# Kernel optimization log

Hardware: AMD Instinct MI355X
Metric: run time of the kernel (lower is better)

Reference implementation:

```python
import jax, jax.numpy as jnp
import numpy as np

N_NODES = 100000
N_EDGES = 1600000
IN_DIM = 3
LATENT = 128
LATENT_DEC = 128
NUM_LAYER = 2      # shared-weight middle GCN layers
NUM_LAYER_DEC = 2  # shared-weight middle decoder layers


def _glorot(key, shape):
    fan_in, fan_out = shape[0], shape[1]
    lim = np.sqrt(6.0 / (fan_in + fan_out)).astype(np.float32)
    return jax.random.uniform(key, shape, jnp.float32, -lim, lim)


def setup_inputs() -> dict:
    key = jax.random.key(0)
    ks = jax.random.split(key, 10)
    x = jax.random.normal(ks[0], (N_NODES, IN_DIM), jnp.float32)
    edge_index = jax.random.randint(ks[1], (2, N_EDGES), 0, N_NODES, jnp.int64)
    return {
        "x": x,
        "edge_index": edge_index,
        "W_s": _glorot(ks[2], (IN_DIM, LATENT)),   "b_s": jnp.zeros((LATENT,), jnp.float32),
        "W_m": _glorot(ks[3], (LATENT, LATENT)),   "b_m": jnp.zeros((LATENT,), jnp.float32),
        "W_e": _glorot(ks[4], (LATENT, LATENT)),   "b_e": jnp.zeros((LATENT,), jnp.float32),
        "W_sd": _glorot(ks[5], (LATENT, LATENT_DEC)),    "b_sd": jnp.zeros((LATENT_DEC,), jnp.float32),
        "W_md": _glorot(ks[6], (LATENT_DEC, LATENT_DEC)),"b_md": jnp.zeros((LATENT_DEC,), jnp.float32),
        "W_ed": _glorot(ks[7], (LATENT_DEC, IN_DIM)),    "b_ed": jnp.zeros((IN_DIM,), jnp.float32),
    }


def _gcn_conv(h, W, b, src, dst, dinv):
    # PyG GCNConv: out_i = sum_j norm_ij * (x_j @ W) + b, norm = d^-1/2_i d^-1/2_j
    h = h @ W
    norm = dinv[src] * dinv[dst]                       # [E+N]
    msg = norm[:, None] * h[src]                       # gather + scale
    out = jax.ops.segment_sum(msg, dst, num_segments=N_NODES)  # scatter-add
    return out + b


def reference(x, edge_index, W_s, b_s, W_m, b_m, W_e, b_e, W_sd, b_sd, W_md, b_md, W_ed, b_ed):
    loops = jnp.arange(N_NODES, dtype=edge_index.dtype)
    src = jnp.concatenate([edge_index[0], loops])      # add self-loops
    dst = jnp.concatenate([edge_index[1], loops])
    deg = jax.ops.segment_sum(jnp.ones(src.shape[0], x.dtype), dst, num_segments=N_NODES)
    dinv = jnp.where(deg > 0, jax.lax.rsqrt(deg), 0.0)

    h = jax.nn.relu(_gcn_conv(x, W_s, b_s, src, dst, dinv))
    for _ in range(NUM_LAYER):  # shared weights (ModuleList([layer]*n))
        h = jax.nn.relu(_gcn_conv(h, W_m, b_m, src, dst, dinv))
    h = jax.nn.relu(_gcn_conv(h, W_e, b_e, src, dst, dinv))

    h = jax.nn.relu(h @ W_sd + b_sd)
    for _ in range(NUM_LAYER_DEC):  # shared weights
        h = jax.nn.relu(h @ W_md + b_md)
    y = h @ W_ed + b_ed
    return y + x
```

## Files before the change

kernel.cpp:

```cpp
#include <hip/hip_runtime.h>


typedef __attribute__((ext_vector_type(8))) short short8;
typedef __attribute__((ext_vector_type(4))) float floatx4;
typedef __attribute__((ext_vector_type(2))) float floatx2;

#define BIN_CH 8192
#define NBMAX 512
#define BKT 256
#define HS_STRIDE 68

__device__ __forceinline__ unsigned short f2bf(float f) {
    unsigned int u = __float_as_uint(f);
    u += 0x7fffu + ((u >> 16) & 1u);
    return (unsigned short)(u >> 16);
}
__device__ __forceinline__ unsigned int pk_bf(float a, float b) {
    return (unsigned int)f2bf(a) | ((unsigned int)f2bf(b) << 16);
}
__device__ __forceinline__ unsigned char f2fp8(float f) {
    return (unsigned char)(__builtin_amdgcn_cvt_pk_fp8_f32(f, f, 0, false) & 0xFF);
}
__device__ __forceinline__ short8 ld_frag(const unsigned short* p) {
    uint2 a = *(const uint2*)p;
    uint2 b = *(const uint2*)(p + 4);
    int4 v = make_int4((int)a.x, (int)a.y, (int)b.x, (int)b.y);
    return __builtin_bit_cast(short8, v);
}


__global__ void pack_kernel(const float* __restrict__ W0, const float* __restrict__ W1,
                            const float* __restrict__ W2, const float* __restrict__ W3,
                            unsigned short* __restrict__ P0, unsigned short* __restrict__ P1,
                            unsigned short* __restrict__ P2, unsigned short* __restrict__ P3,
                            int* __restrict__ gfill, unsigned char* __restrict__ t8zrow,
                            int NB) {
    if (blockIdx.x == 0) {
        for (int i = threadIdx.x; i < NB; i += 256) gfill[i] = 0;
        if (threadIdx.x < 32) ((unsigned int*)t8zrow)[threadIdx.x] = 0;
    }
    int which = blockIdx.x >> 3;
    const float* W = which == 0 ? W0 : which == 1 ? W1 : which == 2 ? W2 : W3;
    unsigned short* P = which == 0 ? P0 : which == 1 ? P1 : which == 2 ? P2 : P3;
    int f = (blockIdx.x & 7) * 256 + threadIdx.x;
    int lane = f & 63, nt = (f >> 6) & 7, kc = f >> 9;
    int kbase = kc * 32 + (lane >> 4) * 8;
    int ncol = nt * 16 + (lane & 15);
    short8 frag;
    #pragma unroll
    for (int j = 0; j < 8; ++j)
        frag[j] = (short)f2bf(W[(size_t)(kbase + j) * 128 + ncol]);
    *((short8*)(P + (size_t)f * 8)) = frag;
}


__global__ __launch_bounds__(512) void bin_kernel(
        const int* __restrict__ src, const int* __restrict__ dst,
        int* __restrict__ gfill, unsigned int* __restrict__ binbuf,
        int NB, int C, int E) {
    __shared__ int h4[4][NBMAX];
    __shared__ int start[NBMAX];
    __shared__ int tot[NBMAX];
    __shared__ int dstoff[NBMAX];
    int tid = threadIdx.x;
    int grp = tid >> 7;
    int e0 = blockIdx.x * BIN_CH;
    for (int i = tid; i < 4 * NBMAX; i += 512) ((int*)h4)[i] = 0;
    __syncthreads();
    for (int i = tid; i < BIN_CH; i += 512) {
        int e = e0 + i;
        if (e < E) atomicAdd(&h4[grp][dst[e] >> 8], 1);
    }
    __syncthreads();
    if (tid < 64) {
        int carry = 0;
        for (int base = 0; base < NB; base += 64) {
            int idx = base + tid;
            int c0 = 0, c1 = 0, c2 = 0, c3 = 0, v = 0;
            if (idx < NB) {
                c0 = h4[0][idx]; c1 = h4[1][idx];
                c2 = h4[2][idx]; c3 = h4[3][idx];
                v = c0 + c1 + c2 + c3;
            }
            int s = v;
            #pragma unroll
            for (int off = 1; off < 64; off <<= 1) {
                int u = __shfl_up(s, off);
                if (tid >= off) s += u;
            }
            if (idx < NB) {
                int ex = carry + s - v;
                start[idx] = ex;
                tot[idx] = v;
                h4[0][idx] = ex;
                h4[1][idx] = ex + c0;
                h4[2][idx] = ex + c0 + c1;
                h4[3][idx] = ex + c0 + c1 + c2;
            }
            carry += __shfl(s, 63);
        }
    }
    __syncthreads();
    for (int i = tid; i < NB; i += 512) {
        int cnt = tot[i];
        int g = cnt ? atomicAdd(&gfill[i], cnt) : 0;
        dstoff[i] = g - start[i];
    }
    __syncthreads();
    for (int i = tid; i < BIN_CH; i += 512) {
        int e = e0 + i;
        if (e >= E) continue;
        int d = dst[e];
        int b = d >> 8;
        int slot = atomicAdd(&h4[grp][b], 1);
        int gidx = b * C + dstoff[b] + slot;
        if (gidx < (b + 1) * C)
            binbuf[gidx] = (unsigned int)src[e] | ((unsigned int)(d & 255) << 17);
    }
}

__global__ __launch_bounds__(256) void build_kernel(
        const unsigned int* __restrict__ binbuf, const int* __restrict__ gfill,
        int* __restrict__ rowptr, float* __restrict__ dinv, int* __restrict__ col,
        int NB, int C, int N, int E) {
    __shared__ int h4[4][BKT];
    __shared__ int hs[BKT];
    __shared__ int tot[BKT];
    __shared__ int bbase_s;
    int b = blockIdx.x, tid = threadIdx.x;
    int grp = tid >> 6;
    int cnt = gfill[b];
    const unsigned int* p = binbuf + (size_t)b * C;
    for (int i = tid; i < 4 * BKT; i += 256) ((int*)h4)[i] = 0;
    __syncthreads();
    if (tid >= 64 && tid < 128) {
        int l = tid - 64;
        int s = 0;
        for (int i = l; i < b; i += 64) s += gfill[i];
        #pragma unroll
        for (int off = 32; off > 0; off >>= 1) s += __shfl_down(s, off);
        if (l == 0) bbase_s = s;
    }
    for (int i = tid; i < cnt; i += 256) atomicAdd(&h4[grp][p[i] >> 17], 1);
    __syncthreads();
    if (tid < 64) {
        int carry = 0;
        for (int base = 0; base < BKT; base += 64) {
            int idx = base + tid;
            int c0 = h4[0][idx], c1 = h4[1][idx], c2 = h4[2][idx], c3 = h4[3][idx];
            int v = c0 + c1 + c2 + c3;
            int s = v;
            #pragma unroll
            for (int off = 1; off < 64; off <<= 1) {
                int u = __shfl_up(s, off);
                if (tid >= off) s += u;
            }
            int ex = carry + s - v;
            hs[idx] = ex;
            tot[idx] = v;
            h4[0][idx] = ex;
            h4[1][idx] = ex + c0;
            h4[2][idx] = ex + c0 + c1;
            h4[3][idx] = ex + c0 + c1 + c2;
            carry += __shfl(s, 63);
        }
    }
    __syncthreads();
    int base = bbase_s;
    if (tid < BKT) {
        int node = b * BKT + tid;
        if (node < N) {
            rowptr[node] = base + hs[tid];
            dinv[node] = 1.0f / sqrtf((float)(tot[tid] + 1));
        }
    }
    if (b == 0 && tid == 0) rowptr[N] = E;
    __syncthreads();
    for (int i = tid; i < cnt; i += 256) {
        unsigned int u = p[i];
        int local = u >> 17;
        int pos = atomicAdd(&h4[grp][local], 1);
        col[base + pos] = (int)(u & 0x1FFFFu);
    }
}


__global__ void in_gemm_kernel(const float* __restrict__ x, const float* __restrict__ W,
                               const float* __restrict__ dinv,
                               unsigned char* __restrict__ t8, int n) {
    int g = blockIdx.x * 256 + threadIdx.x;
    int i = g >> 6, c2 = g & 63;
    if (i >= n) return;
    float x0 = x[i * 3], x1 = x[i * 3 + 1], x2 = x[i * 3 + 2];
    float d = dinv[i];
    int c = c2 * 2;
    float v0 = d * (x0 * W[c]     + x1 * W[128 + c]     + x2 * W[256 + c]);
    float v1 = d * (x0 * W[c + 1] + x1 * W[128 + c + 1] + x2 * W[256 + c + 1]);
    unsigned int pk = __builtin_amdgcn_cvt_pk_fp8_f32(v0, v1, 0, false);
    ((unsigned short*)t8)[(size_t)i * 64 + c2] = (unsigned short)(pk & 0xFFFF);
}


__global__ __launch_bounds__(256) void agg_kernel(
        const unsigned char* __restrict__ t8, const int* __restrict__ rowptr,
        const int* __restrict__ col, const float* __restrict__ dinv,
        const float* __restrict__ bias, unsigned short* __restrict__ out, int n) {
    int node = blockIdx.x * 16 + (threadIdx.x >> 4);
    int lane = threadIdx.x & 63;
    int q16 = lane >> 4;
    int lq  = lane & 15;
    int oct = (lane >> 3) & 1;
    int l8  = lane & 7;
    if (node >= n) node = n - 1;
    floatx2 acc[8];
    #pragma unroll
    for (int i = 0; i < 8; ++i) acc[i] = (floatx2){0.f, 0.f};

    int beg = rowptr[node];
    int deg = rowptr[node + 1] - beg;
    for (int base = 0; base < deg; base += 32) {
        int m = deg - base;
        int jv0 = (lq < m)      ? col[beg + base + lq]      : n;
        int jv1 = (lq + 16 < m) ? col[beg + base + 16 + lq] : n;
        uint4 v[16];
        #pragma unroll
        for (int q = 0; q < 8; ++q) {
            int j = __shfl(jv0, q16 * 16 + q * 2 + oct);
            v[q] = ((const uint4*)(t8 + (size_t)j * 128))[l8];
        }
        #pragma unroll
        for (int q = 0; q < 8; ++q) {
            int j = __shfl(jv1, q16 * 16 + q * 2 + oct);
            v[8 + q] = ((const uint4*)(t8 + (size_t)j * 128))[l8];
        }
        #pragma unroll
        for (int q = 0; q < 16; ++q) {
            acc[0] += __builtin_amdgcn_cvt_pk_f32_fp8(v[q].x, false);
            acc[1] += __builtin_amdgcn_cvt_pk_f32_fp8(v[q].x, true);
            acc[2] += __builtin_amdgcn_cvt_pk_f32_fp8(v[q].y, false);
            acc[3] += __builtin_amdgcn_cvt_pk_f32_fp8(v[q].y, true);
            acc[4] += __builtin_amdgcn_cvt_pk_f32_fp8(v[q].z, false);
            acc[5] += __builtin_amdgcn_cvt_pk_f32_fp8(v[q].z, true);
            acc[6] += __builtin_amdgcn_cvt_pk_f32_fp8(v[q].w, false);
            acc[7] += __builtin_amdgcn_cvt_pk_f32_fp8(v[q].w, true);
        }
    }
    #pragma unroll
    for (int i = 0; i < 8; ++i) {
        acc[i].x += __shfl_xor(acc[i].x, 8);
        acc[i].y += __shfl_xor(acc[i].y, 8);
    }
    uint4 s = ((const uint4*)(t8 + (size_t)node * 128))[l8];
    acc[0] += __builtin_amdgcn_cvt_pk_f32_fp8(s.x, false);
    acc[1] += __builtin_amdgcn_cvt_pk_f32_fp8(s.x, true);
    acc[2] += __builtin_amdgcn_cvt_pk_f32_fp8(s.y, false);
    acc[3] += __builtin_amdgcn_cvt_pk_f32_fp8(s.y, true);
    acc[4] += __builtin_amdgcn_cvt_pk_f32_fp8(s.z, false);
    acc[5] += __builtin_amdgcn_cvt_pk_f32_fp8(s.z, true);
    acc[6] += __builtin_amdgcn_cvt_pk_f32_fp8(s.w, false);
    acc[7] += __builtin_amdgcn_cvt_pk_f32_fp8(s.w, true);

    float di = dinv[node];
    const float4* b4 = (const float4*)bias;
    float o[16];
    #pragma unroll
    for (int k = 0; k < 4; ++k) {
        float4 bb = b4[l8 * 4 + k];
        o[k*4+0] = fmaxf(di * acc[k*2].x   + bb.x, 0.f);
        o[k*4+1] = fmaxf(di * acc[k*2].y   + bb.y, 0.f);
        o[k*4+2] = fmaxf(di * acc[k*2+1].x + bb.z, 0.f);
        o[k*4+3] = fmaxf(di * acc[k*2+1].y + bb.w, 0.f);
    }
    if (oct == 0) {
        uint4 w0, w1;
        w0.x = pk_bf(o[0],  o[1]);  w0.y = pk_bf(o[2],  o[3]);
        w0.z = pk_bf(o[4],  o[5]);  w0.w = pk_bf(o[6],  o[7]);
        w1.x = pk_bf(o[8],  o[9]);  w1.y = pk_bf(o[10], o[11]);
        w1.z = pk_bf(o[12], o[13]); w1.w = pk_bf(o[14], o[15]);
        ((uint4*)(out + (size_t)node * 128))[l8 * 2]     = w0;
        ((uint4*)(out + (size_t)node * 128))[l8 * 2 + 1] = w1;
    }
}


__device__ __forceinline__ void gemm_regs(const short8 af[2][4], const unsigned short* Ws,
                                          int lane, floatx4 acc[2][8]) {
    #pragma unroll
    for (int t = 0; t < 2; ++t)
        #pragma unroll
        for (int nt = 0; nt < 8; ++nt) acc[t][nt] = (floatx4){0.f, 0.f, 0.f, 0.f};
    #pragma unroll
    for (int kc = 0; kc < 4; ++kc) {
        #pragma unroll
        for (int nt = 0; nt < 8; ++nt) {
            short8 bf = *((const short8*)(Ws + ((kc * 8 + nt) * 64 + lane) * 8));
            acc[0][nt] = __builtin_amdgcn_mfma_f32_16x16x32_bf16(af[0][kc], bf, acc[0][nt], 0, 0, 0);
            acc[1][nt] = __builtin_amdgcn_mfma_f32_16x16x32_bf16(af[1][kc], bf, acc[1][nt], 0, 0, 0);
        }
    }
}

__device__ __forceinline__ void gemm_lds(const unsigned short* Hs, const unsigned short* Ws,
                                         int wav, int lane, floatx4 acc[2][8]) {
    int quad = lane >> 4, mrow = lane & 15;
    short8 af[2][4];
    #pragma unroll
    for (int t = 0; t < 2; ++t)
        #pragma unroll
        for (int kc = 0; kc < 4; ++kc)
            af[t][kc] = ld_frag(Hs + (wav * 32 + t * 16 + mrow) * HS_STRIDE + (kc * 4 + quad) * 8);
    gemm_regs(af, Ws, lane, acc);
}

__device__ __forceinline__ void relu_store_hs(
        unsigned short* Hs, const float* __restrict__ bias,
        floatx4 acc[2][8], int wav, int lane) {
    int quad = lane >> 4, mrow = lane & 15;
    #pragma unroll
    for (int t = 0; t < 2; ++t) {
        #pragma unroll
        for (int nt = 0; nt < 8; ++nt) {
            int colc = nt * 16 + mrow;
            float bcol = bias[colc];
            #pragma unroll
            for (int r = 0; r < 4; ++r) {
                int rowl = wav * 32 + t * 16 + quad * 4 + r;
                Hs[rowl * HS_STRIDE + colc] = f2bf(fmaxf(acc[t][nt][r] + bcol, 0.f));
            }
        }
    }
}


__global__ __launch_bounds__(256, 4) void gemm_enc_kernel(
        const unsigned short* __restrict__ A, const unsigned short* __restrict__ Wp,
        const float* __restrict__ dinv, unsigned char* __restrict__ outp, int n) {
    int tid = threadIdx.x;
    int wave = tid >> 6, lane = tid & 63;
    int quad = lane >> 4, mrow = lane & 15;
    int row0 = blockIdx.x * 128 + wave * 32;

    short8 af[2][4];
    #pragma unroll
    for (int t = 0; t < 2; ++t) {
        int arow = row0 + t * 16 + mrow; if (arow >= n) arow = n - 1;
        const unsigned short* abase = A + (size_t)arow * 128 + quad * 8;
        #pragma unroll
        for (int kc = 0; kc < 4; ++kc)
            af[t][kc] = *((const short8*)(abase + kc * 32));
    }
    floatx4 acc[2][8];
    gemm_regs(af, Wp, lane, acc);

    #pragma unroll
    for (int t = 0; t < 2; ++t) {
        int rbase = row0 + t * 16 + quad * 4;
        float dv[4];
        #pragma unroll
        for (int r = 0; r < 4; ++r)
            dv[r] = (rbase + r < n) ? dinv[rbase + r] : 0.f;
        #pragma unroll
        for (int nt = 0; nt < 8; ++nt) {
            int colc = nt * 16 + mrow;
            #pragma unroll
            for (int r = 0; r < 4; ++r) {
                int row = rbase + r;
                if (row < n)
                    outp[(size_t)row * 128 + colc] = f2fp8(acc[t][nt][r] * dv[r]);
            }
        }
    }
}


__global__ __launch_bounds__(256, 4) void decoder_kernel(
        const unsigned short* __restrict__ A,
        const unsigned short* __restrict__ Wp_sd, const float* __restrict__ b_sd,
        const unsigned short* __restrict__ Wp_md, const float* __restrict__ b_md,
        const float* __restrict__ W_ed, const float* __restrict__ b_ed,
        const float* __restrict__ x, float* __restrict__ out, int n) {
    __shared__ unsigned short Hs[128 * HS_STRIDE];
    int tid = threadIdx.x;
    int wav = tid >> 6, lane = tid & 63;
    int quad = lane >> 4, mrow = lane & 15;
    int row0 = blockIdx.x * 128 + wav * 32;

    short8 af[2][4];
    #pragma unroll
    for (int t = 0; t < 2; ++t) {
        int arow = row0 + t * 16 + mrow; if (arow >= n) arow = n - 1;
        const unsigned short* abase = A + (size_t)arow * 128 + quad * 8;
        #pragma unroll
        for (int kc = 0; kc < 4; ++kc)
            af[t][kc] = *((const short8*)(abase + kc * 32));
    }

    floatx4 acc[2][8];
    gemm_regs(af, Wp_sd, lane, acc);
    relu_store_hs(Hs, b_sd, acc, wav, lane);
    gemm_lds(Hs, Wp_md, wav, lane, acc);
    relu_store_hs(Hs, b_md, acc, wav, lane);
    gemm_lds(Hs, Wp_md, wav, lane, acc);

    float wed[8][3];
    #pragma unroll
    for (int nt = 0; nt < 8; ++nt) {
        int c = nt * 16 + mrow;
        #pragma unroll
        for (int k = 0; k < 3; ++k) wed[nt][k] = W_ed[c * 3 + k];
    }
    #pragma unroll
    for (int t = 0; t < 2; ++t) {
        #pragma unroll
        for (int r = 0; r < 4; ++r) {
            float s0 = 0.f, s1 = 0.f, s2 = 0.f;
            #pragma unroll
            for (int nt = 0; nt < 8; ++nt) {
                float v = fmaxf(acc[t][nt][r] + b_md[nt * 16 + mrow], 0.f);
                s0 += v * wed[nt][0]; s1 += v * wed[nt][1]; s2 += v * wed[nt][2];
            }
            #pragma unroll
            for (int off = 1; off < 16; off <<= 1) {
                s0 += __shfl_xor(s0, off);
                s1 += __shfl_xor(s1, off);
                s2 += __shfl_xor(s2, off);
            }
            if (mrow == 0) {
                int row = row0 + t * 16 + quad * 4 + r;
                if (row < n) {
                    out[row * 3 + 0] = s0 + b_ed[0] + x[row * 3 + 0];
                    out[row * 3 + 1] = s1 + b_ed[1] + x[row * 3 + 1];
                    out[row * 3 + 2] = s2 + b_ed[2] + x[row * 3 + 2];
                }
            }
        }
    }
}


extern "C" void kernel_launch(void* const* d_in, const int* in_sizes, int n_in,
                              void* d_out, int out_size, void* d_ws, size_t ws_size,
                              hipStream_t stream) {
    const float* x    = (const float*)d_in[0];
    const int*   ei   = (const int*)d_in[1];
    const float* W_s  = (const float*)d_in[2];
    const float* b_s  = (const float*)d_in[3];
    const float* W_m  = (const float*)d_in[4];
    const float* b_m  = (const float*)d_in[5];
    const float* W_e  = (const float*)d_in[6];
    const float* b_e  = (const float*)d_in[7];
    const float* W_sd = (const float*)d_in[8];
    const float* b_sd = (const float*)d_in[9];
    const float* W_md = (const float*)d_in[10];
    const float* b_md = (const float*)d_in[11];
    const float* W_ed = (const float*)d_in[12];
    const float* b_ed = (const float*)d_in[13];
    float* outp = (float*)d_out;

    const int N = in_sizes[0] / 3;
    const int E = in_sizes[1] / 2;
    const int* src = ei;
    const int* dst = ei + E;

    const int NB = (N + BKT - 1) / BKT;
    const int C  = (((E / NB) * 3 / 2) + 255) & ~255;

    char* p = (char*)d_ws;
    auto carve = [&](size_t bytes) {
        void* r = (void*)p;
        p += (bytes + 255) & ~(size_t)255;
        return r;
    };
    int*   rowptr = (int*)  carve((size_t)(N + 1) * 4);
    int*   col    = (int*)  carve((size_t)E * 4);
    float* dinv   = (float*)carve((size_t)N * 4);
    int*   gfill  = (int*)  carve((size_t)NB * 4);
    unsigned int* binbuf = (unsigned int*)carve((size_t)NB * C * 4);
    unsigned short* Wp_m  = (unsigned short*)carve(16384 * 2);
    unsigned short* Wp_e  = (unsigned short*)carve(16384 * 2);
    unsigned short* Wp_sd = (unsigned short*)carve(16384 * 2);
    unsigned short* Wp_md = (unsigned short*)carve(16384 * 2);
    unsigned char*  T8 = (unsigned char*) carve((size_t)(N + 1) * 128);
    unsigned short* A  = (unsigned short*)carve((size_t)N * 128 * 2);
    (void)ws_size;

    const int gBin = (E + BIN_CH - 1) / BIN_CH;
    const int gNode16 = (N + 15) / 16;
    const int gRow128 = (N + 127) / 128;

    pack_kernel<<<32, 256, 0, stream>>>(W_m, W_e, W_sd, W_md, Wp_m, Wp_e, Wp_sd, Wp_md,
                                        gfill, T8 + (size_t)N * 128, NB);

    bin_kernel<<<gBin, 512, 0, stream>>>(src, dst, gfill, binbuf, NB, C, E);
    build_kernel<<<NB, 256, 0, stream>>>(binbuf, gfill, rowptr, dinv, col, NB, C, N, E);

    in_gemm_kernel<<<(N * 64 + 255) / 256, 256, 0, stream>>>(x, W_s, dinv, T8, N);
    agg_kernel<<<gNode16, 256, 0, stream>>>(T8, rowptr, col, dinv, b_s, A, N);
    gemm_enc_kernel<<<gRow128, 256, 0, stream>>>(A, Wp_m, dinv, T8, N);
    agg_kernel<<<gNode16, 256, 0, stream>>>(T8, rowptr, col, dinv, b_m, A, N);
    gemm_enc_kernel<<<gRow128, 256, 0, stream>>>(A, Wp_m, dinv, T8, N);
    agg_kernel<<<gNode16, 256, 0, stream>>>(T8, rowptr, col, dinv, b_m, A, N);
    gemm_enc_kernel<<<gRow128, 256, 0, stream>>>(A, Wp_e, dinv, T8, N);
    agg_kernel<<<gNode16, 256, 0, stream>>>(T8, rowptr, col, dinv, b_e, A, N);

    decoder_kernel<<<gRow128, 256, 0, stream>>>(A, Wp_sd, b_sd, Wp_md, b_md,
                                                W_ed, b_ed, x, outp, N);
}
```

Before: 374.5 us.

## Fuse neighbor aggregation with following GEMM via LDS staging and ping-pong buffers

Aggregation now writes each 128-row block's bf16 result into shared memory, and the next layer's MFMA GEMM (or the whole decoder) reads it from there in the same kernel. This removes the global bf16 intermediate array A and its write/read round trip, and cuts the launch count. Two fp8 feature buffers are used ping-pong because blocks read neighbor rows while other blocks write new features. The trade-off is coarser per-block work: 128 nodes per block with 8 serial nodes per 16-lane group, plus lower occupancy (launch bounds 256,3), which may reduce latency hiding for the irregular gathers.

```diff
diff --git a/kernel.cpp b/kernel.cpp
--- a/kernel.cpp
+++ b/kernel.cpp
@@ -33,11 +33,14 @@
                             const float* __restrict__ W2, const float* __restrict__ W3,
                             unsigned short* __restrict__ P0, unsigned short* __restrict__ P1,
                             unsigned short* __restrict__ P2, unsigned short* __restrict__ P3,
-                            int* __restrict__ gfill, unsigned char* __restrict__ t8zrow,
-                            int NB) {
+                            int* __restrict__ gfill, unsigned char* __restrict__ t8zrowA,
+                            unsigned char* __restrict__ t8zrowB, int NB) {
     if (blockIdx.x == 0) {
         for (int i = threadIdx.x; i < NB; i += 256) gfill[i] = 0;
-        if (threadIdx.x < 32) ((unsigned int*)t8zrow)[threadIdx.x] = 0;
+        if (threadIdx.x < 32) {
+            ((unsigned int*)t8zrowA)[threadIdx.x] = 0;
+            ((unsigned int*)t8zrowB)[threadIdx.x] = 0;
+        }
     }
     int which = blockIdx.x >> 3;
     const float* W = which == 0 ? W0 : which == 1 ? W1 : which == 2 ? W2 : W3;
@@ -201,156 +204,161 @@
 }
 
 
-__global__ __launch_bounds__(256) void agg_kernel(
+__device__ __forceinline__ void gemm_regs(const short8 af[2][4], const unsigned short* Ws,
+                                          int lane, floatx4 acc[2][8]) {
+    #pragma unroll
+    for (int t = 0; t < 2; ++t)
+        #pragma unroll
+        for (int nt = 0; nt < 8; ++nt) acc[t][nt] = (floatx4){0.f, 0.f, 0.f, 0.f};
+    #pragma unroll
+    for (int kc = 0; kc < 4; ++kc) {
+        #pragma unroll
+        for (int nt = 0; nt < 8; ++nt) {
+            short8 bf = *((const short8*)(Ws + ((kc * 8 + nt) * 64 + lane) * 8));
+            acc[0][nt] = __builtin_amdgcn_mfma_f32_16x16x32_bf16(af[0][kc], bf, acc[0][nt], 0, 0, 0);
+            acc[1][nt] = __builtin_amdgcn_mfma_f32_16x16x32_bf16(af[1][kc], bf, acc[1][nt], 0, 0, 0);
+        }
+    }
+}
+
+__device__ __forceinline__ void gemm_lds(const unsigned short* Hs, const unsigned short* Ws,
+                                         int wav, int lane, floatx4 acc[2][8]) {
+    int quad = lane >> 4, mrow = lane & 15;
+    short8 af[2][4];
+    #pragma unroll
+    for (int t = 0; t < 2; ++t)
+        #pragma unroll
+        for (int kc = 0; kc < 4; ++kc)
+            af[t][kc] = ld_frag(Hs + (wav * 32 + t * 16 + mrow) * HS_STRIDE + (kc * 4 + quad) * 8);
+    gemm_regs(af, Ws, lane, acc);
+}
+
+__device__ __forceinline__ void relu_store_hs(
+        unsigned short* Hs, const float* __restrict__ bias,
+        floatx4 acc[2][8], int wav, int lane) {
+    int quad = lane >> 4, mrow = lane & 15;
+    #pragma unroll
+    for (int t = 0; t < 2; ++t) {
+        #pragma unroll
+        for (int nt = 0; nt < 8; ++nt) {
+            int colc = nt * 16 + mrow;
+            float bcol = bias[colc];
+            #pragma unroll
+            for (int r = 0; r < 4; ++r) {
+                int rowl = wav * 32 + t * 16 + quad * 4 + r;
+                Hs[rowl * HS_STRIDE + colc] = f2bf(fmaxf(acc[t][nt][r] + bcol, 0.f));
+            }
+        }
+    }
+}
+
+
+__device__ __forceinline__ void agg_to_hs(
         const unsigned char* __restrict__ t8, const int* __restrict__ rowptr,
         const int* __restrict__ col, const float* __restrict__ dinv,
-        const float* __restrict__ bias, unsigned short* __restrict__ out, int n) {
-    int node = blockIdx.x * 16 + (threadIdx.x >> 4);
-    int lane = threadIdx.x & 63;
+        const float* __restrict__ bias, unsigned short* Hs, int n) {
+    int tid = threadIdx.x;
+    int lane = tid & 63;
     int q16 = lane >> 4;
     int lq  = lane & 15;
     int oct = (lane >> 3) & 1;
     int l8  = lane & 7;
-    if (node >= n) node = n - 1;
-    floatx2 acc[8];
-    #pragma unroll
-    for (int i = 0; i < 8; ++i) acc[i] = (floatx2){0.f, 0.f};
-
-    int beg = rowptr[node];
-    int deg = rowptr[node + 1] - beg;
-    for (int base = 0; base < deg; base += 32) {
-        int m = deg - base;
-        int jv0 = (lq < m)      ? col[beg + base + lq]      : n;
-        int jv1 = (lq + 16 < m) ? col[beg + base + 16 + lq] : n;
-        uint4 v[16];
-        #pragma unroll
-        for (int q = 0; q < 8; ++q) {
-            int j = __shfl(jv0, q16 * 16 + q * 2 + oct);
-            v[q] = ((const uint4*)(t8 + (size_t)j * 128))[l8];
-        }
-        #pragma unroll
-        for (int q = 0; q < 8; ++q) {
-            int j = __shfl(jv1, q16 * 16 + q * 2 + oct);
-            v[8 + q] = ((const uint4*)(t8 + (size_t)j * 128))[l8];
-        }
-        #pragma unroll
-        for (int q = 0; q < 16; ++q) {
-            acc[0] += __builtin_amdgcn_cvt_pk_f32_fp8(v[q].x, false);
-            acc[1] += __builtin_amdgcn_cvt_pk_f32_fp8(v[q].x, true);
-            acc[2] += __builtin_amdgcn_cvt_pk_f32_fp8(v[q].y, false);
-            acc[3] += __builtin_amdgcn_cvt_pk_f32_fp8(v[q].y, true);
-            acc[4] += __builtin_amdgcn_cvt_pk_f32_fp8(v[q].z, false);
-            acc[5] += __builtin_amdgcn_cvt_pk_f32_fp8(v[q].z, true);
-            acc[6] += __builtin_amdgcn_cvt_pk_f32_fp8(v[q].w, false);
-            acc[7] += __builtin_amdgcn_cvt_pk_f32_fp8(v[q].w, true);
-        }
-    }
-    #pragma unroll
-    for (int i = 0; i < 8; ++i) {
-        acc[i].x += __shfl_xor(acc[i].x, 8);
-        acc[i].y += __shfl_xor(acc[i].y, 8);
-    }
-    uint4 s = ((const uint4*)(t8 + (size_t)node * 128))[l8];
-    acc[0] += __builtin_amdgcn_cvt_pk_f32_fp8(s.x, false);
-    acc[1] += __builtin_amdgcn_cvt_pk_f32_fp8(s.x, true);
-    acc[2] += __builtin_amdgcn_cvt_pk_f32_fp8(s.y, false);
-    acc[3] += __builtin_amdgcn_cvt_pk_f32_fp8(s.y, true);
-    acc[4] += __builtin_amdgcn_cvt_pk_f32_fp8(s.z, false);
-    acc[5] += __builtin_amdgcn_cvt_pk_f32_fp8(s.z, true);
-    acc[6] += __builtin_amdgcn_cvt_pk_f32_fp8(s.w, false);
-    acc[7] += __builtin_amdgcn_cvt_pk_f32_fp8(s.w, true);
-
-    float di = dinv[node];
+    int qrow0 = (tid >> 4) * 8;
     const float4* b4 = (const float4*)bias;
-    float o[16];
-    #pragma unroll
-    for (int k = 0; k < 4; ++k) {
-        float4 bb = b4[l8 * 4 + k];
-        o[k*4+0] = fmaxf(di * acc[k*2].x   + bb.x, 0.f);
-        o[k*4+1] = fmaxf(di * acc[k*2].y   + bb.y, 0.f);
-        o[k*4+2] = fmaxf(di * acc[k*2+1].x + bb.z, 0.f);
-        o[k*4+3] = fmaxf(di * acc[k*2+1].y + bb.w, 0.f);
-    }
-    if (oct == 0) {
-        uint4 w0, w1;
-        w0.x = pk_bf(o[0],  o[1]);  w0.y = pk_bf(o[2],  o[3]);
-        w0.z = pk_bf(o[4],  o[5]);  w0.w = pk_bf(o[6],  o[7]);
-        w1.x = pk_bf(o[8],  o[9]);  w1.y = pk_bf(o[10], o[11]);
-        w1.z = pk_bf(o[12], o[13]); w1.w = pk_bf(o[14], o[15]);
-        ((uint4*)(out + (size_t)node * 128))[l8 * 2]     = w0;
-        ((uint4*)(out + (size_t)node * 128))[l8 * 2 + 1] = w1;
-    }
-}
-
-
-__device__ __forceinline__ void gemm_regs(const short8 af[2][4], const unsigned short* Ws,
-                                          int lane, floatx4 acc[2][8]) {
-    #pragma unroll
-    for (int t = 0; t < 2; ++t)
-        #pragma unroll
-        for (int nt = 0; nt < 8; ++nt) acc[t][nt] = (floatx4){0.f, 0.f, 0.f, 0.f};
-    #pragma unroll
-    for (int kc = 0; kc < 4; ++kc) {
-        #pragma unroll
-        for (int nt = 0; nt < 8; ++nt) {
-            short8 bf = *((const short8*)(Ws + ((kc * 8 + nt) * 64 + lane) * 8));
-            acc[0][nt] = __builtin_amdgcn_mfma_f32_16x16x32_bf16(af[0][kc], bf, acc[0][nt], 0, 0, 0);
-            acc[1][nt] = __builtin_amdgcn_mfma_f32_16x16x32_bf16(af[1][kc], bf, acc[1][nt], 0, 0, 0);
-        }
-    }
-}
-
-__device__ __forceinline__ void gemm_lds(const unsigned short* Hs, const unsigned short* Ws,
-                                         int wav, int lane, floatx4 acc[2][8]) {
+
+    for (int it = 0; it < 8; ++it) {
+        int rowl = qrow0 + it;
+        int node = blockIdx.x * 128 + rowl;
+        if (node >= n) node = n - 1;
+        floatx2 acc[8];
+        #pragma unroll
+        for (int i = 0; i < 8; ++i) acc[i] = (floatx2){0.f, 0.f};
+
+        int beg = rowptr[node];
+        int deg = rowptr[node + 1] - beg;
+        for (int base = 0; base < deg; base += 32) {
+            int m = deg - base;
+            int jv0 = (lq < m)      ? col[beg + base + lq]      : n;
+            int jv1 = (lq + 16 < m) ? col[beg + base + 16 + lq] : n;
+            uint4 v[16];
+            #pragma unroll
+            for (int q = 0; q < 8; ++q) {
+                int j = __shfl(jv0, q16 * 16 + q * 2 + oct);
+                v[q] = ((const uint4*)(t8 + (size_t)j * 128))[l8];
+            }
+            #pragma unroll
+            for (int q = 0; q < 8; ++q) {
+                int j = __shfl(jv1, q16 * 16 + q * 2 + oct);
+                v[8 + q] = ((const uint4*)(t8 + (size_t)j * 128))[l8];
+            }
+            #pragma unroll
+            for (int q = 0; q < 16; ++q) {
+                acc[0] += __builtin_amdgcn_cvt_pk_f32_fp8(v[q].x, false);
+                acc[1] += __builtin_amdgcn_cvt_pk_f32_fp8(v[q].x, true);
+                acc[2] += __builtin_amdgcn_cvt_pk_f32_fp8(v[q].y, false);
+                acc[3] += __builtin_amdgcn_cvt_pk_f32_fp8(v[q].y, true);
+                acc[4] += __builtin_amdgcn_cvt_pk_f32_fp8(v[q].z, false);
+                acc[5] += __builtin_amdgcn_cvt_pk_f32_fp8(v[q].z, true);
+                acc[6] += __builtin_amdgcn_cvt_pk_f32_fp8(v[q].w, false);
+                acc[7] += __builtin_amdgcn_cvt_pk_f32_fp8(v[q].w, true);
+            }
+        }
+        #pragma unroll
+        for (int i = 0; i < 8; ++i) {
+            acc[i].x += __shfl_xor(acc[i].x, 8);
+            acc[i].y += __shfl_xor(acc[i].y, 8);
+        }
+        uint4 s = ((const uint4*)(t8 + (size_t)node * 128))[l8];
+        acc[0] += __builtin_amdgcn_cvt_pk_f32_fp8(s.x, false);
+        acc[1] += __builtin_amdgcn_cvt_pk_f32_fp8(s.x, true);
+        acc[2] += __builtin_amdgcn_cvt_pk_f32_fp8(s.y, false);
+        acc[3] += __builtin_amdgcn_cvt_pk_f32_fp8(s.y, true);
+        acc[4] += __builtin_amdgcn_cvt_pk_f32_fp8(s.z, false);
+        acc[5] += __builtin_amdgcn_cvt_pk_f32_fp8(s.z, true);
+        acc[6] += __builtin_amdgcn_cvt_pk_f32_fp8(s.w, false);
+        acc[7] += __builtin_amdgcn_cvt_pk_f32_fp8(s.w, true);
+
+        float di = dinv[node];
+        float o[16];
+        #pragma unroll
+        for (int k = 0; k < 4; ++k) {
+            float4 bb = b4[l8 * 4 + k];
+            o[k*4+0] = fmaxf(di * acc[k*2].x   + bb.x, 0.f);
+            o[k*4+1] = fmaxf(di * acc[k*2].y   + bb.y, 0.f);
+            o[k*4+2] = fmaxf(di * acc[k*2+1].x + bb.z, 0.f);
+            o[k*4+3] = fmaxf(di * acc[k*2+1].y + bb.w, 0.f);
+        }
+        if (oct == 0) {
+            unsigned short* hp = Hs + rowl * HS_STRIDE + l8 * 16;
+            uint2 w;
+            w.x = pk_bf(o[0],  o[1]);  w.y = pk_bf(o[2],  o[3]);
+            *(uint2*)(hp)     = w;
+            w.x = pk_bf(o[4],  o[5]);  w.y = pk_bf(o[6],  o[7]);
+            *(uint2*)(hp + 4) = w;
+            w.x = pk_bf(o[8],  o[9]);  w.y = pk_bf(o[10], o[11]);
+            *(uint2*)(hp + 8) = w;
+            w.x = pk_bf(o[12], o[13]); w.y = pk_bf(o[14], o[15]);
+            *(uint2*)(hp + 12) = w;
+        }
+    }
+}
+
+
+__global__ __launch_bounds__(256, 3) void agg_gemm_kernel(
+        const unsigned char* __restrict__ t8, const int* __restrict__ rowptr,
+        const int* __restrict__ col, const float* __restrict__ dinv,
+        const float* __restrict__ bias, const unsigned short* __restrict__ Wp,
+        unsigned char* __restrict__ outp, int n) {
+    __shared__ unsigned short Hs[128 * HS_STRIDE];
+    agg_to_hs(t8, rowptr, col, dinv, bias, Hs, n);
+
+    int tid = threadIdx.x;
+    int wav = tid >> 6, lane = tid & 63;
     int quad = lane >> 4, mrow = lane & 15;
-    short8 af[2][4];
-    #pragma unroll
-    for (int t = 0; t < 2; ++t)
-        #pragma unroll
-        for (int kc = 0; kc < 4; ++kc)
-            af[t][kc] = ld_frag(Hs + (wav * 32 + t * 16 + mrow) * HS_STRIDE + (kc * 4 + quad) * 8);
-    gemm_regs(af, Ws, lane, acc);
-}
-
-__device__ __forceinline__ void relu_store_hs(
-        unsigned short* Hs, const float* __restrict__ bias,
-        floatx4 acc[2][8], int wav, int lane) {
-    int quad = lane >> 4, mrow = lane & 15;
-    #pragma unroll
-    for (int t = 0; t < 2; ++t) {
-        #pragma unroll
-        for (int nt = 0; nt < 8; ++nt) {
-            int colc = nt * 16 + mrow;
-            float bcol = bias[colc];
-            #pragma unroll
-            for (int r = 0; r < 4; ++r) {
-                int rowl = wav * 32 + t * 16 + quad * 4 + r;
-                Hs[rowl * HS_STRIDE + colc] = f2bf(fmaxf(acc[t][nt][r] + bcol, 0.f));
-            }
-        }
-    }
-}
-
-
-__global__ __launch_bounds__(256, 4) void gemm_enc_kernel(
-        const unsigned short* __restrict__ A, const unsigned short* __restrict__ Wp,
-        const float* __restrict__ dinv, unsigned char* __restrict__ outp, int n) {
-    int tid = threadIdx.x;
-    int wave = tid >> 6, lane = tid & 63;
-    int quad = lane >> 4, mrow = lane & 15;
-    int row0 = blockIdx.x * 128 + wave * 32;
-
-    short8 af[2][4];
-    #pragma unroll
-    for (int t = 0; t < 2; ++t) {
-        int arow = row0 + t * 16 + mrow; if (arow >= n) arow = n - 1;
-        const unsigned short* abase = A + (size_t)arow * 128 + quad * 8;
-        #pragma unroll
-        for (int kc = 0; kc < 4; ++kc)
-            af[t][kc] = *((const short8*)(abase + kc * 32));
-    }
+    int row0 = blockIdx.x * 128 + wav * 32;
+
     floatx4 acc[2][8];
-    gemm_regs(af, Wp, lane, acc);
+    gemm_lds(Hs, Wp, wav, lane, acc);
 
     #pragma unroll
     for (int t = 0; t < 2; ++t) {
@@ -373,30 +381,24 @@
 }
 
 
-__global__ __launch_bounds__(256, 4) void decoder_kernel(
-        const unsigned short* __restrict__ A,
+__global__ __launch_bounds__(256, 3) void agg_dec_kernel(
+        const unsigned char* __restrict__ t8, const int* __restrict__ rowptr,
+        const int* __restrict__ col, const float* __restrict__ dinv,
+        const float* __restrict__ bias,
         const unsigned short* __restrict__ Wp_sd, const float* __restrict__ b_sd,
         const unsigned short* __restrict__ Wp_md, const float* __restrict__ b_md,
         const float* __restrict__ W_ed, const float* __restrict__ b_ed,
         const float* __restrict__ x, float* __restrict__ out, int n) {
     __shared__ unsigned short Hs[128 * HS_STRIDE];
+    agg_to_hs(t8, rowptr, col, dinv, bias, Hs, n);
+
     int tid = threadIdx.x;
     int wav = tid >> 6, lane = tid & 63;
     int quad = lane >> 4, mrow = lane & 15;
     int row0 = blockIdx.x * 128 + wav * 32;
 
-    short8 af[2][4];
-    #pragma unroll
-    for (int t = 0; t < 2; ++t) {
-        int arow = row0 + t * 16 + mrow; if (arow >= n) arow = n - 1;
-        const unsigned short* abase = A + (size_t)arow * 128 + quad * 8;
-        #pragma unroll
-        for (int kc = 0; kc < 4; ++kc)
-            af[t][kc] = *((const short8*)(abase + kc * 32));
-    }
-
     floatx4 acc[2][8];
-    gemm_regs(af, Wp_sd, lane, acc);
+    gemm_lds(Hs, Wp_sd, wav, lane, acc);
     relu_store_hs(Hs, b_sd, acc, wav, lane);
     gemm_lds(Hs, Wp_md, wav, lane, acc);
     relu_store_hs(Hs, b_md, acc, wav, lane);
@@ -480,29 +482,26 @@
     unsigned short* Wp_e  = (unsigned short*)carve(16384 * 2);
     unsigned short* Wp_sd = (unsigned short*)carve(16384 * 2);
     unsigned short* Wp_md = (unsigned short*)carve(16384 * 2);
-    unsigned char*  T8 = (unsigned char*) carve((size_t)(N + 1) * 128);
-    unsigned short* A  = (unsigned short*)carve((size_t)N * 128 * 2);
+    unsigned char*  T8a = (unsigned char*) carve((size_t)(N + 1) * 128);
+    unsigned char*  T8b = (unsigned char*) carve((size_t)(N + 1) * 128);
     (void)ws_size;
 
     const int gBin = (E + BIN_CH - 1) / BIN_CH;
-    const int gNode16 = (N + 15) / 16;
     const int gRow128 = (N + 127) / 128;
 
     pack_kernel<<<32, 256, 0, stream>>>(W_m, W_e, W_sd, W_md, Wp_m, Wp_e, Wp_sd, Wp_md,
-                                        gfill, T8 + (size_t)N * 128, NB);
+                                        gfill, T8a + (size_t)N * 128,
+                                        T8b + (size_t)N * 128, NB);
 
     bin_kernel<<<gBin, 512, 0, stream>>>(src, dst, gfill, binbuf, NB, C, E);
     build_kernel<<<NB, 256, 0, stream>>>(binbuf, gfill, rowptr, dinv, col, NB, C, N, E);
 
-    in_gemm_kernel<<<(N * 64 + 255) / 256, 256, 0, stream>>>(x, W_s, dinv, T8, N);
-    agg_kernel<<<gNode16, 256, 0, stream>>>(T8, rowptr, col, dinv, b_s, A, N);
-    gemm_enc_kernel<<<gRow128, 256, 0, stream>>>(A, Wp_m, dinv, T8, N);
-    agg_kernel<<<gNode16, 256, 0, stream>>>(T8, rowptr, col, dinv, b_m, A, N);
-    gemm_enc_kernel<<<gRow128, 256, 0, stream>>>(A, Wp_m, dinv, T8, N);
-    agg_kernel<<<gNode16, 256, 0, stream>>>(T8, rowptr, col, dinv, b_m, A, N);
-    gemm_enc_kernel<<<gRow128, 256, 0, stream>>>(A, Wp_e, dinv, T8, N);
-    agg_kernel<<<gNode16, 256, 0, stream>>>(T8, rowptr, col, dinv, b_e, A, N);
-
-    decoder_kernel<<<gRow128, 256, 0, stream>>>(A, Wp_sd, b_sd, Wp_md, b_md,
+    in_gemm_kernel<<<(N * 64 + 255) / 256, 256, 0, stream>>>(x, W_s, dinv, T8a, N);
+    agg_gemm_kernel<<<gRow128, 256, 0, stream>>>(T8a, rowptr, col, dinv, b_s, Wp_m, T8b, N);
+    agg_gemm_kernel<<<gRow128, 256, 0, stream>>>(T8b, rowptr, col, dinv, b_m, Wp_m, T8a, N);
+    agg_gemm_kernel<<<gRow128, 256, 0, stream>>>(T8a, rowptr, col, dinv, b_m, Wp_e, T8b, N);
+
+    agg_dec_kernel<<<gRow128, 256, 0, stream>>>(T8b, rowptr, col, dinv, b_e,
+                                                Wp_sd, b_sd, Wp_md, b_md,
                                                 W_ed, b_ed, x, outp, N);
 }
```

After: 372.9 us. Within noise of the previous version (-0.4%).
